# Kernel optimization log

Hardware: AMD Instinct MI355X
Metric: run time of the kernel (lower is better)

## Reference

```python
import jax, jax.numpy as jnp
import numpy as np

D_MODEL = 1024
NUM_HEADS = 16
D_K = D_MODEL // NUM_HEADS


def setup_inputs() -> dict:
    key = jax.random.key(0)
    ks = jax.random.split(key, 9)
    s = 1.0 / np.sqrt(D_MODEL)
    inp = {
        "x": jax.random.normal(ks[0], (2, 2048, D_MODEL), dtype=jnp.float32),
        "Wq": jax.random.uniform(ks[1], (D_MODEL, D_MODEL), jnp.float32, -s, s),
        "bq": jax.random.uniform(ks[2], (D_MODEL,), jnp.float32, -s, s),
        "Wk": jax.random.uniform(ks[3], (D_MODEL, D_MODEL), jnp.float32, -s, s),
        "bk": jax.random.uniform(ks[4], (D_MODEL,), jnp.float32, -s, s),
        "Wv": jax.random.uniform(ks[5], (D_MODEL, D_MODEL), jnp.float32, -s, s),
        "bv": jax.random.uniform(ks[6], (D_MODEL,), jnp.float32, -s, s),
        "Wo": jax.random.uniform(ks[7], (D_MODEL, D_MODEL), jnp.float32, -s, s),
        "bo": jax.random.uniform(ks[8], (D_MODEL,), jnp.float32, -s, s),
    }
    return inp


def reference(x, Wq, bq, Wk, bk, Wv, bv, Wo, bo):
    B, S, _ = x.shape
    # projections (torch Linear: y = x @ W.T + b)
    q = x @ Wq.T + bq
    k = x @ Wk.T + bk
    v = x @ Wv.T + bv
    # [B, H, S, Dk]
    q = q.reshape(B, S, NUM_HEADS, D_K).transpose(0, 2, 1, 3)
    k = k.reshape(B, S, NUM_HEADS, D_K).transpose(0, 2, 1, 3)
    v = v.reshape(B, S, NUM_HEADS, D_K).transpose(0, 2, 1, 3)
    scale = 1.0 / np.sqrt(D_K).astype(np.float32)
    energy = jnp.einsum("bhqd,bhkd->bhqk", q, k) * scale
    attn = jax.nn.softmax(energy, axis=-1)
    out = jnp.einsum("bhqk,bhkd->bhqd", attn, v)
    out = out.transpose(0, 2, 1, 3).reshape(B, S, D_MODEL)
    return out @ Wo.T + bo
```

## Files before the change

### kernel.cpp

```cpp
#include <hip/hip_runtime.h>
#include <hip/hip_bf16.h>
#include <cstdint>

typedef __bf16 bf16;
typedef __bf16 bf16x4 __attribute__((ext_vector_type(4)));
typedef __bf16 bf16x8 __attribute__((ext_vector_type(8)));
typedef float f32x4 __attribute__((ext_vector_type(4)));
typedef float f32x16 __attribute__((ext_vector_type(16)));
typedef unsigned int u32x4 __attribute__((ext_vector_type(4)));

#define DM   1024
#define SEQ  2048
#define NH   16
#define DKH  64

__device__ __forceinline__ bf16x8 ld8(const bf16* p) {
    return *reinterpret_cast<const bf16x8*>(p);
}

__device__ __forceinline__ void gld16(const void* g, void* lds) {
    __builtin_amdgcn_global_load_lds(
        (__attribute__((address_space(1))) void*)(uintptr_t)g,
        (__attribute__((address_space(3))) void*)(uint32_t)(uintptr_t)lds,
        16, 0, 0);
}

__device__ __forceinline__ f32x4 mfma16(bf16x8 a, bf16x8 b, f32x4 c) {
    return __builtin_amdgcn_mfma_f32_16x16x32_bf16(a, b, c, 0, 0, 0);
}
__device__ __forceinline__ f32x16 mfma32(bf16x8 a, bf16x8 b, f32x16 c) {
    return __builtin_amdgcn_mfma_f32_32x32x16_bf16(a, b, c, 0, 0, 0);
}

__device__ __forceinline__ unsigned pkbf(float lo, float hi) {
    unsigned r;
    asm("v_cvt_pk_bf16_f32 %0, %1, %2" : "=v"(r) : "v"(lo), "v"(hi));
    return r;
}
__device__ __forceinline__ void plswap(unsigned& a, unsigned& b) {
    asm volatile("v_permlane32_swap_b32 %0, %1" : "+v"(a), "+v"(b));
}

__global__ __launch_bounds__(256) void cvt_all(
    const float4* __restrict__ x,  const float4* __restrict__ wq,
    const float4* __restrict__ wk, const float4* __restrict__ wv,
    const float4* __restrict__ wo,
    ushort4* __restrict__ xb,  ushort4* __restrict__ wqb,
    ushort4* __restrict__ wkb, ushort4* __restrict__ wvb,
    ushort4* __restrict__ wob) {
    int i = blockIdx.x * 256 + threadIdx.x;
    const float4* src;
    ushort4* dst;
    int off;
    if (i < 1048576) {
        src = x; dst = xb; off = i;
    } else {
        int r = i - 1048576;
        int sel = r >> 18;
        off = r & 262143;
        src = sel == 0 ? wq : sel == 1 ? wk : sel == 2 ? wv : wo;
        dst = sel == 0 ? wqb : sel == 1 ? wkb : sel == 2 ? wvb : wob;
    }
    float4 f = src[off];
    ushort4 u;
    u.x = __builtin_bit_cast(unsigned short, (bf16)f.x);
    u.y = __builtin_bit_cast(unsigned short, (bf16)f.y);
    u.z = __builtin_bit_cast(unsigned short, (bf16)f.z);
    u.w = __builtin_bit_cast(unsigned short, (bf16)f.w);
    dst[off] = u;
}

template <int OUT_MODE>
__device__ __forceinline__ void gemm_body(const bf16* __restrict__ A,
                                          const bf16* __restrict__ W,
                                          const float* __restrict__ bias,
                                          void* __restrict__ outp,
                                          int m0, int n0, float scale,
                                          bf16* __restrict__ As,
                                          bf16* __restrict__ Bs) {
    constexpr int K = DM, BK = 64;

    const int t     = threadIdx.x;
    const int lane  = t & 63;
    const int row16 = lane & 15, grp = lane >> 4;
    const int wave  = t >> 6;
    const int wr    = (wave >> 1) * 64;
    const int wc    = (wave & 1) * 64;

    f32x4 acc[4][4] = {};

    const int sc = (t & 7) * 8;
    const bf16* Ag = A + (size_t)(m0 + (t >> 3)) * K + sc;
    const bf16* Wg = W + (size_t)(n0 + (t >> 3)) * K + sc;
    bf16* Asw = &As[t * 8];
    bf16* Bsw = &Bs[t * 8];

    for (int kt = 0; kt < K; kt += BK) {
        __syncthreads();
#pragma unroll
        for (int i = 0; i < 4; ++i) {
            gld16(Ag + (size_t)i * 32 * K + kt, Asw + i * 2048);
            gld16(Wg + (size_t)i * 32 * K + kt, Bsw + i * 2048);
        }
        __syncthreads();
#pragma unroll
        for (int kk = 0; kk < BK; kk += 32) {
            bf16x8 af[4], bfr[4];
#pragma unroll
            for (int m = 0; m < 4; ++m)
                af[m] = ld8(&As[(wr + m * 16 + row16) * BK + kk + grp * 8]);
#pragma unroll
            for (int n = 0; n < 4; ++n)
                bfr[n] = ld8(&Bs[(wc + n * 16 + row16) * BK + kk + grp * 8]);
#pragma unroll
            for (int m = 0; m < 4; ++m)
#pragma unroll
                for (int n = 0; n < 4; ++n)
                    acc[m][n] = mfma16(af[m], bfr[n], acc[m][n]);
        }
    }

    if constexpr (OUT_MODE == 2) {
        __syncthreads();
        bf16* Tw = (wave < 2) ? As + wave * 4096 : Bs + (wave - 2) * 4096;
        const int b = m0 >> 11;
        const int tokbase = (m0 & 2047) + wr;
#pragma unroll
        for (int n = 0; n < 4; ++n) {
            const int dim = n * 16 + row16;
            const float bv = bias[n0 + wc + dim];
#pragma unroll
            for (int m = 0; m < 4; ++m) {
                bf16x4 w4 = {(bf16)(acc[m][n][0] + bv), (bf16)(acc[m][n][1] + bv),
                             (bf16)(acc[m][n][2] + bv), (bf16)(acc[m][n][3] + bv)};
                const int slot = (m * 2 + (grp >> 1)) ^ (dim & 7);
                *reinterpret_cast<bf16x4*>(&Tw[dim * 64 + slot * 8 + (grp & 1) * 4]) = w4;
            }
        }
        asm volatile("" ::: "memory");
#pragma unroll
        for (int r = 0; r < 8; ++r) {
            const int dim = (lane >> 3) + 8 * r;
            const int ts  = lane & 7;
            bf16x8 v = ld8(&Tw[dim * 64 + ((ts ^ (dim & 7)) * 8)]);
            const int col = n0 + wc + dim;
            bf16* dst = (bf16*)outp +
                ((size_t)(b * NH + (col >> 6)) * DKH + (col & 63)) * SEQ +
                tokbase + ts * 8;
            *reinterpret_cast<bf16x8*>(dst) = v;
        }
    } else {
#pragma unroll
        for (int n = 0; n < 4; ++n) {
            const int col = n0 + wc + n * 16 + row16;
            const float bv = bias[col];
#pragma unroll
            for (int m = 0; m < 4; ++m) {
                const int row = m0 + wr + m * 16 + grp * 4;
#pragma unroll
                for (int j = 0; j < 4; ++j) {
                    float v = (acc[m][n][j] + bv) * scale;
                    if constexpr (OUT_MODE == 1)
                        ((float*)outp)[(size_t)(row + j) * DM + col] = v;
                    else
                        ((bf16*)outp)[(size_t)(row + j) * DM + col] = (bf16)v;
                }
            }
        }
    }
}

__global__ __launch_bounds__(256, 4) void gemm_qkv(
    const bf16* __restrict__ xb,
    const bf16* __restrict__ wqb, const bf16* __restrict__ wkb, const bf16* __restrict__ wvb,
    const float* __restrict__ bq, const float* __restrict__ bk, const float* __restrict__ bv,
    bf16* __restrict__ q, bf16* __restrict__ k, bf16* __restrict__ vt) {
    __shared__ __attribute__((aligned(16))) bf16 As[128 * 64];
    __shared__ __attribute__((aligned(16))) bf16 Bs[128 * 64];
    const int sel = blockIdx.y >> 3;
    const int m0 = blockIdx.x * 128, n0 = (blockIdx.y & 7) * 128;
    if (sel == 0) {
        gemm_body<0>(xb, wqb, bq, q, m0, n0, 0.18033688f, As, Bs);
    } else if (sel == 1) {
        gemm_body<0>(xb, wkb, bk, k, m0, n0, 1.0f, As, Bs);
    } else {
        gemm_body<2>(xb, wvb, bv, vt, m0, n0, 1.0f, As, Bs);
    }
}

__global__ __launch_bounds__(256, 4) void gemm_out(
    const bf16* __restrict__ ab, const bf16* __restrict__ wob,
    const float* __restrict__ bo, float* __restrict__ out) {
    __shared__ __attribute__((aligned(16))) bf16 As[128 * 64];
    __shared__ __attribute__((aligned(16))) bf16 Bs[128 * 64];
    gemm_body<1>(ab, wob, bo, out, blockIdx.x * 128, blockIdx.y * 128, 1.0f, As, Bs);
}

__global__ __launch_bounds__(256) void attn(const bf16* __restrict__ Q,
                                            const bf16* __restrict__ K,
                                            const bf16* __restrict__ VT,
                                            bf16* __restrict__ O) {
    __shared__ __attribute__((aligned(16))) bf16 Ks[2][64 * 64];
    __shared__ __attribute__((aligned(16))) bf16 Vs[2][64 * 64];

    const int t = threadIdx.x, lane = t & 63, wave = t >> 6;
    const int l31 = lane & 31, hi = lane >> 5;

    int id = blockIdx.x;
    id = (id & 7) * 64 + (id >> 3);
    const int qt = id & 15, h = (id >> 4) & 15, b = id >> 8;

    const bf16* Qb = Q + ((size_t)b * SEQ + qt * 128) * DM + h * DKH;
    const bf16* Kb = K + (size_t)b * SEQ * DM + h * DKH;
    const bf16* Vb = VT + (size_t)((b * NH + h) * DKH) * SEQ;

    bf16x8 qf[4];
#pragma unroll
    for (int c = 0; c < 4; ++c)
        qf[c] = ld8(Qb + (size_t)(wave * 32 + l31) * DM + c * 16 + hi * 8);

    f32x16 o[2] = {};
    float L = 0.f;

    const int sr = t >> 3, scs = t & 7;

    auto STAGE = [&](int bsel, int kt) {
#pragma unroll
        for (int i = 0; i < 2; ++i) {
            const int r = i * 32 + sr;
            const int cs = (scs ^ (r & 7)) * 8;
            gld16(Kb + (size_t)(kt + r) * DM + cs, &Ks[bsel][i * 2048 + t * 8]);
            gld16(Vb + (size_t)r * SEQ + kt + cs, &Vs[bsel][i * 2048 + t * 8]);
        }
    };

    STAGE(0, 0);
    __syncthreads();

    int cur = 0;
    for (int kt = 0; kt < SEQ; kt += 64) {
        if (kt + 64 < SEQ) STAGE(cur ^ 1, kt + 64);
        const bf16* KsB = Ks[cur];
        const bf16* VsB = Vs[cur];

        u32x4 up[4];
#pragma unroll
        for (int sub = 0; sub < 2; ++sub) {
            const int krow = sub * 32 + l31;
            const int ksw  = krow & 7;
            f32x16 ss = {};
            __builtin_amdgcn_s_setprio(1);
#pragma unroll
            for (int c = 0; c < 4; ++c) {
                const bf16x8 kf = ld8(&KsB[krow * 64 + (((c * 2 + hi) ^ ksw) * 8)]);
                ss = mfma32(kf, qf[c], ss);
            }
            __builtin_amdgcn_s_setprio(0);
            float e[16];
#pragma unroll
            for (int r = 0; r < 16; ++r) {
                e[r] = __builtin_amdgcn_exp2f(ss[r]);
                L += e[r];
            }
            unsigned u0 = pkbf(e[0],  e[1]),  u1 = pkbf(e[2],  e[3]);
            unsigned u2 = pkbf(e[4],  e[5]),  u3 = pkbf(e[6],  e[7]);
            unsigned u4 = pkbf(e[8],  e[9]),  u5 = pkbf(e[10], e[11]);
            unsigned u6 = pkbf(e[12], e[13]), u7 = pkbf(e[14], e[15]);
            plswap(u0, u2); plswap(u1, u3);
            plswap(u4, u6); plswap(u5, u7);
            up[sub * 2]     = u32x4{u0, u1, u2, u3};
            up[sub * 2 + 1] = u32x4{u4, u5, u6, u7};
        }

        __builtin_amdgcn_s_setprio(1);
#pragma unroll
        for (int dt = 0; dt < 2; ++dt) {
            const int vrow = dt * 32 + l31;
            const int vsw  = vrow & 7;
#pragma unroll
            for (int kc = 0; kc < 4; ++kc) {
                const bf16x8 vf = ld8(&VsB[vrow * 64 + (((kc * 2 + hi) ^ vsw) * 8)]);
                o[dt] = mfma32(__builtin_bit_cast(bf16x8, up[kc]), vf, o[dt]);
            }
        }
        __builtin_amdgcn_s_setprio(0);

        __syncthreads();
        cur ^= 1;
    }

    const float Lfull = L + __shfl_xor(L, 32);
    const float inv = 1.0f / Lfull;
    float invr[16];
#pragma unroll
    for (int r = 0; r < 16; ++r)
        invr[r] = __shfl(inv, (r & 3) + 8 * (r >> 2) + 4 * hi);
#pragma unroll
    for (int dt = 0; dt < 2; ++dt)
#pragma unroll
        for (int r = 0; r < 16; ++r) {
            const int ql = (r & 3) + 8 * (r >> 2) + 4 * hi;
            O[((size_t)b * SEQ + qt * 128 + wave * 32 + ql) * DM
              + h * DKH + dt * 32 + l31] = (bf16)(o[dt][r] * invr[r]);
        }
}

extern "C" void kernel_launch(void* const* d_in, const int* in_sizes, int n_in,
                              void* d_out, int out_size, void* d_ws, size_t ws_size,
                              hipStream_t stream) {
    const float* x  = (const float*)d_in[0];
    const float* Wq = (const float*)d_in[1];
    const float* bq = (const float*)d_in[2];
    const float* Wk = (const float*)d_in[3];
    const float* bk = (const float*)d_in[4];
    const float* Wv = (const float*)d_in[5];
    const float* bv = (const float*)d_in[6];
    const float* Wo = (const float*)d_in[7];
    const float* bo = (const float*)d_in[8];
    float* out = (float*)d_out;

    char* ws = (char*)d_ws;
    bf16* xb  = (bf16*)(ws + 0);
    bf16* wqb = (bf16*)(ws + 8388608);
    bf16* wkb = (bf16*)(ws + 10485760);
    bf16* wvb = (bf16*)(ws + 12582912);
    bf16* wob = (bf16*)(ws + 14680064);
    bf16* qb  = (bf16*)(ws + 16777216);
    bf16* kb  = (bf16*)(ws + 25165824);
    bf16* ab  = (bf16*)(ws + 33554432);
    bf16* vtb = (bf16*)(ws + 41943040);

    cvt_all<<<8192, 256, 0, stream>>>(
        (const float4*)x, (const float4*)Wq, (const float4*)Wk,
        (const float4*)Wv, (const float4*)Wo,
        (ushort4*)xb, (ushort4*)wqb, (ushort4*)wkb, (ushort4*)wvb, (ushort4*)wob);

    gemm_qkv<<<dim3(32, 24), 256, 0, stream>>>(xb, wqb, wkb, wvb, bq, bk, bv, qb, kb, vtb);

    attn<<<dim3(512), 256, 0, stream>>>(qb, kb, vtb, ab);

    gemm_out<<<dim3(32, 8), 256, 0, stream>>>(ab, wob, bo, out);
}
```

Before: 122.8 us.

## Rewrite QKV GEMM as 256x256 tile, double-buffered, swizzled LDS kernel

The fused QKV projection becomes a single 512-thread kernel with 256x256 output tiles over a concatenated Wq/Wk/Wv weight matrix, giving 192 blocks. Global-to-LDS loads are double-buffered with explicit vmcnt waits so the next K-tile's copy overlaps the current MFMAs. An XOR swizzle reduces LDS bank conflicts, and setprio raises priority around the MFMA block. The larger tile raises arithmetic intensity, but the 192-block grid may underfill the GPU's CUs and the kernel holds more registers and LDS per block.

```diff
diff --git a/kernel.cpp b/kernel.cpp
--- a/kernel.cpp
+++ b/kernel.cpp
@@ -70,15 +70,141 @@
     dst[off] = u;
 }
 
-template <int OUT_MODE>
-__device__ __forceinline__ void gemm_body(const bf16* __restrict__ A,
-                                          const bf16* __restrict__ W,
-                                          const float* __restrict__ bias,
-                                          void* __restrict__ outp,
-                                          int m0, int n0, float scale,
-                                          bf16* __restrict__ As,
-                                          bf16* __restrict__ Bs) {
+__global__ __launch_bounds__(512, 2) void gemm_qkv(
+    const bf16* __restrict__ A,
+    const bf16* __restrict__ W,
+    const float* __restrict__ bq, const float* __restrict__ bk,
+    const float* __restrict__ bv_,
+    bf16* __restrict__ q, bf16* __restrict__ k, bf16* __restrict__ vt) {
+    __shared__ __attribute__((aligned(16))) bf16 S[69632];
+
+    const int t    = threadIdx.x;
+    const int lane = t & 63;
+    const int r16  = lane & 15, grp = lane >> 4;
+    const int wave = t >> 6;
+    const int wr   = (wave >> 2) * 128;
+    const int wc   = (wave & 3) * 64;
+
+    int id = blockIdx.x;
+    id = (id & 7) * 24 + (id >> 3);
+    const int m0 = (id & 15) * 256;
+    const int n0 = (id >> 4) * 256;
+
+    f32x4 acc[8][4] = {};
+
+    const int srow = t >> 3;
+    const int scol = t & 7;
+
+    auto STAGE = [&](int buf, int kt) {
+#pragma unroll
+        for (int i = 0; i < 4; ++i) {
+            const int row = i * 64 + srow;
+            const int cs = ((scol ^ (row & 7)) * 8);
+            gld16(A + (size_t)(m0 + row) * DM + kt * 64 + cs,
+                  &S[buf * 32768 + i * 4096 + t * 8]);
+            gld16(W + (size_t)(n0 + row) * DM + kt * 64 + cs,
+                  &S[buf * 32768 + 16384 + i * 4096 + t * 8]);
+        }
+    };
+
+    STAGE(0, 0);
+    STAGE(1, 1);
+
+    for (int kt = 0; kt < 16; ++kt) {
+        if (kt == 15) { asm volatile("s_waitcnt vmcnt(0)" ::: "memory"); }
+        else         { asm volatile("s_waitcnt vmcnt(8)" ::: "memory"); }
+        __builtin_amdgcn_sched_barrier(0);
+        __builtin_amdgcn_s_barrier();
+
+        const int cur = kt & 1;
+        const bf16* Ab = &S[cur * 32768];
+        const bf16* Bb = &S[cur * 32768 + 16384];
+#pragma unroll
+        for (int kk = 0; kk < 2; ++kk) {
+            const int sl = kk * 4 + grp;
+            bf16x8 af[8], bf[4];
+#pragma unroll
+            for (int m = 0; m < 8; ++m) {
+                const int row = wr + m * 16 + r16;
+                af[m] = ld8(&Ab[row * 64 + ((sl ^ (row & 7)) * 8)]);
+            }
+#pragma unroll
+            for (int n = 0; n < 4; ++n) {
+                const int row = wc + n * 16 + r16;
+                bf[n] = ld8(&Bb[row * 64 + ((sl ^ (row & 7)) * 8)]);
+            }
+            __builtin_amdgcn_s_setprio(1);
+#pragma unroll
+            for (int m = 0; m < 8; ++m)
+#pragma unroll
+                for (int n = 0; n < 4; ++n)
+                    acc[m][n] = mfma16(af[m], bf[n], acc[m][n]);
+            __builtin_amdgcn_s_setprio(0);
+        }
+
+        __builtin_amdgcn_sched_barrier(0);
+        __builtin_amdgcn_s_barrier();
+        __builtin_amdgcn_sched_barrier(0);
+        if (kt + 2 < 16) STAGE(cur, kt + 2);
+    }
+
+    if (n0 < 2048) {
+        const float scale = (n0 < 1024) ? 0.18033688f : 1.0f;
+        bf16* out = (n0 < 1024) ? q : k;
+        const float* bias = (n0 < 1024) ? bq : bk;
+        const int nc0 = n0 & 1023;
+#pragma unroll
+        for (int n = 0; n < 4; ++n) {
+            const int col = nc0 + wc + n * 16 + r16;
+            const float bvv = bias[col];
+#pragma unroll
+            for (int m = 0; m < 8; ++m) {
+                const int row = m0 + wr + m * 16 + grp * 4;
+#pragma unroll
+                for (int j = 0; j < 4; ++j)
+                    out[(size_t)(row + j) * DM + col] =
+                        (bf16)((acc[m][n][j] + bvv) * scale);
+            }
+        }
+    } else {
+        const int nc0 = n0 - 2048;
+        const int b = m0 >> 11;
+        const int s0 = (m0 & 2047) + wr;
+        bf16* Tw = &S[wave * 8704];
+#pragma unroll
+        for (int n = 0; n < 4; ++n) {
+            const int dl = n * 16 + r16;
+            const float bvv = bv_[nc0 + wc + dl];
+#pragma unroll
+            for (int m = 0; m < 8; ++m) {
+                bf16x4 w4 = {(bf16)(acc[m][n][0] + bvv), (bf16)(acc[m][n][1] + bvv),
+                             (bf16)(acc[m][n][2] + bvv), (bf16)(acc[m][n][3] + bvv)};
+                *reinterpret_cast<bf16x4*>(&Tw[dl * 136 + m * 16 + grp * 4]) = w4;
+            }
+        }
+        asm volatile("" ::: "memory");
+#pragma unroll
+        for (int dd = 0; dd < 8; ++dd) {
+            const int dim = dd * 8 + (lane >> 3);
+            const int col = nc0 + wc + dim;
+            const int h = col >> 6, d = col & 63;
+            bf16* dst = vt + ((size_t)(b * NH + h) * DKH + d) * SEQ + s0;
+#pragma unroll
+            for (int cc = 0; cc < 2; ++cc) {
+                const int c = (lane & 7) + cc * 8;
+                bf16x8 v = ld8(&Tw[dim * 136 + c * 8]);
+                *reinterpret_cast<bf16x8*>(dst + c * 8) = v;
+            }
+        }
+    }
+}
+
+__global__ __launch_bounds__(256, 4) void gemm_out(
+    const bf16* __restrict__ A, const bf16* __restrict__ W,
+    const float* __restrict__ bias, float* __restrict__ out) {
     constexpr int K = DM, BK = 64;
+    __shared__ __attribute__((aligned(16))) bf16 As[128 * BK];
+    __shared__ __attribute__((aligned(16))) bf16 Bs[128 * BK];
 
     const int t     = threadIdx.x;
     const int lane  = t & 63;
@@ -86,6 +212,7 @@
     const int wave  = t >> 6;
     const int wr    = (wave >> 1) * 64;
     const int wc    = (wave & 1) * 64;
+    const int m0 = blockIdx.x * 128, n0 = blockIdx.y * 128;
 
     f32x4 acc[4][4] = {};
 
@@ -120,80 +247,18 @@
         }
     }
 
-    if constexpr (OUT_MODE == 2) {
-        __syncthreads();
-        bf16* Tw = (wave < 2) ? As + wave * 4096 : Bs + (wave - 2) * 4096;
-        const int b = m0 >> 11;
-        const int tokbase = (m0 & 2047) + wr;
-#pragma unroll
-        for (int n = 0; n < 4; ++n) {
-            const int dim = n * 16 + row16;
-            const float bv = bias[n0 + wc + dim];
-#pragma unroll
-            for (int m = 0; m < 4; ++m) {
-                bf16x4 w4 = {(bf16)(acc[m][n][0] + bv), (bf16)(acc[m][n][1] + bv),
-                             (bf16)(acc[m][n][2] + bv), (bf16)(acc[m][n][3] + bv)};
-                const int slot = (m * 2 + (grp >> 1)) ^ (dim & 7);
-                *reinterpret_cast<bf16x4*>(&Tw[dim * 64 + slot * 8 + (grp & 1) * 4]) = w4;
-            }
-        }
-        asm volatile("" ::: "memory");
-#pragma unroll
-        for (int r = 0; r < 8; ++r) {
-            const int dim = (lane >> 3) + 8 * r;
-            const int ts  = lane & 7;
-            bf16x8 v = ld8(&Tw[dim * 64 + ((ts ^ (dim & 7)) * 8)]);
-            const int col = n0 + wc + dim;
-            bf16* dst = (bf16*)outp +
-                ((size_t)(b * NH + (col >> 6)) * DKH + (col & 63)) * SEQ +
-                tokbase + ts * 8;
-            *reinterpret_cast<bf16x8*>(dst) = v;
-        }
-    } else {
-#pragma unroll
-        for (int n = 0; n < 4; ++n) {
-            const int col = n0 + wc + n * 16 + row16;
-            const float bv = bias[col];
-#pragma unroll
-            for (int m = 0; m < 4; ++m) {
-                const int row = m0 + wr + m * 16 + grp * 4;
-#pragma unroll
-                for (int j = 0; j < 4; ++j) {
-                    float v = (acc[m][n][j] + bv) * scale;
-                    if constexpr (OUT_MODE == 1)
-                        ((float*)outp)[(size_t)(row + j) * DM + col] = v;
-                    else
-                        ((bf16*)outp)[(size_t)(row + j) * DM + col] = (bf16)v;
-                }
-            }
-        }
-    }
-}
-
-__global__ __launch_bounds__(256, 4) void gemm_qkv(
-    const bf16* __restrict__ xb,
-    const bf16* __restrict__ wqb, const bf16* __restrict__ wkb, const bf16* __restrict__ wvb,
-    const float* __restrict__ bq, const float* __restrict__ bk, const float* __restrict__ bv,
-    bf16* __restrict__ q, bf16* __restrict__ k, bf16* __restrict__ vt) {
-    __shared__ __attribute__((aligned(16))) bf16 As[128 * 64];
-    __shared__ __attribute__((aligned(16))) bf16 Bs[128 * 64];
-    const int sel = blockIdx.y >> 3;
-    const int m0 = blockIdx.x * 128, n0 = (blockIdx.y & 7) * 128;
-    if (sel == 0) {
-        gemm_body<0>(xb, wqb, bq, q, m0, n0, 0.18033688f, As, Bs);
-    } else if (sel == 1) {
-        gemm_body<0>(xb, wkb, bk, k, m0, n0, 1.0f, As, Bs);
-    } else {
-        gemm_body<2>(xb, wvb, bv, vt, m0, n0, 1.0f, As, Bs);
-    }
-}
-
-__global__ __launch_bounds__(256, 4) void gemm_out(
-    const bf16* __restrict__ ab, const bf16* __restrict__ wob,
-    const float* __restrict__ bo, float* __restrict__ out) {
-    __shared__ __attribute__((aligned(16))) bf16 As[128 * 64];
-    __shared__ __attribute__((aligned(16))) bf16 Bs[128 * 64];
-    gemm_body<1>(ab, wob, bo, out, blockIdx.x * 128, blockIdx.y * 128, 1.0f, As, Bs);
+#pragma unroll
+    for (int n = 0; n < 4; ++n) {
+        const int col = n0 + wc + n * 16 + row16;
+        const float bvv = bias[col];
+#pragma unroll
+        for (int m = 0; m < 4; ++m) {
+            const int row = m0 + wr + m * 16 + grp * 4;
+#pragma unroll
+            for (int j = 0; j < 4; ++j)
+                out[(size_t)(row + j) * DM + col] = acc[m][n][j] + bvv;
+        }
+    }
 }
 
 __global__ __launch_bounds__(256) void attn(const bf16* __restrict__ Q,
@@ -320,22 +385,23 @@
     float* out = (float*)d_out;
 
     char* ws = (char*)d_ws;
-    bf16* xb  = (bf16*)(ws + 0);
-    bf16* wqb = (bf16*)(ws + 8388608);
-    bf16* wkb = (bf16*)(ws + 10485760);
-    bf16* wvb = (bf16*)(ws + 12582912);
-    bf16* wob = (bf16*)(ws + 14680064);
-    bf16* qb  = (bf16*)(ws + 16777216);
-    bf16* kb  = (bf16*)(ws + 25165824);
-    bf16* ab  = (bf16*)(ws + 33554432);
-    bf16* vtb = (bf16*)(ws + 41943040);
+    bf16* xb   = (bf16*)(ws + 0);
+    bf16* wqkv = (bf16*)(ws + 8388608);
+    bf16* wqb  = (bf16*)(ws + 8388608);
+    bf16* wkb  = (bf16*)(ws + 10485760);
+    bf16* wvb  = (bf16*)(ws + 12582912);
+    bf16* wob  = (bf16*)(ws + 14680064);
+    bf16* qb   = (bf16*)(ws + 16777216);
+    bf16* kb   = (bf16*)(ws + 25165824);
+    bf16* ab   = (bf16*)(ws + 33554432);
+    bf16* vtb  = (bf16*)(ws + 41943040);
 
     cvt_all<<<8192, 256, 0, stream>>>(
         (const float4*)x, (const float4*)Wq, (const float4*)Wk,
         (const float4*)Wv, (const float4*)Wo,
         (ushort4*)xb, (ushort4*)wqb, (ushort4*)wkb, (ushort4*)wvb, (ushort4*)wob);
 
-    gemm_qkv<<<dim3(32, 24), 256, 0, stream>>>(xb, wqb, wkb, wvb, bq, bk, bv, qb, kb, vtb);
+    gemm_qkv<<<192, 512, 0, stream>>>(xb, wqkv, bq, bk, bv, qb, kb, vtb);
 
     attn<<<dim3(512), 256, 0, stream>>>(qb, kb, vtb, ab);
 
```

Result: faster. 119.2 us (-2.9%).

## Triple-buffer GEMM K-loop with async LDS loads, swizzle and block remap

Applied to the files above, without the earlier changes.

Rewrites the shared GEMM body as a three-stage pipelined K-loop with BK=32. It uses global_load_lds prefetches two tiles ahead, partial vmcnt waits and a single barrier per step, so global loads overlap MFMA work. The LDS rows get an XOR swizzle against bank conflicts, and MFMA sections are wrapped in raised wave priority. The QKV GEMM now treats the contiguous Wq/Wk/Wv buffers as one fused weight matrix, and both GEMMs use a 1D grid with an XCD-aware block remap. The larger LDS footprint lowers the occupancy hint from 4 to 3 blocks per CU.

```diff
diff --git a/kernel.cpp b/kernel.cpp
--- a/kernel.cpp
+++ b/kernel.cpp
@@ -76,63 +76,80 @@
                                           const float* __restrict__ bias,
                                           void* __restrict__ outp,
                                           int m0, int n0, float scale,
-                                          bf16* __restrict__ As,
-                                          bf16* __restrict__ Bs) {
-    constexpr int K = DM, BK = 64;
-
-    const int t     = threadIdx.x;
-    const int lane  = t & 63;
-    const int row16 = lane & 15, grp = lane >> 4;
-    const int wave  = t >> 6;
-    const int wr    = (wave >> 1) * 64;
-    const int wc    = (wave & 1) * 64;
+                                          bf16* __restrict__ S) {
+    constexpr int BK = 32;
+    const int t    = threadIdx.x;
+    const int lane = t & 63;
+    const int r16  = lane & 15, grp = lane >> 4;
+    const int wave = t >> 6;
+    const int wr   = (wave >> 1) * 64;
+    const int wc   = (wave & 1) * 64;
 
     f32x4 acc[4][4] = {};
 
-    const int sc = (t & 7) * 8;
-    const bf16* Ag = A + (size_t)(m0 + (t >> 3)) * K + sc;
-    const bf16* Wg = W + (size_t)(n0 + (t >> 3)) * K + sc;
-    bf16* Asw = &As[t * 8];
-    bf16* Bsw = &Bs[t * 8];
-
-    for (int kt = 0; kt < K; kt += BK) {
-        __syncthreads();
-#pragma unroll
-        for (int i = 0; i < 4; ++i) {
-            gld16(Ag + (size_t)i * 32 * K + kt, Asw + i * 2048);
-            gld16(Wg + (size_t)i * 32 * K + kt, Bsw + i * 2048);
-        }
-        __syncthreads();
-#pragma unroll
-        for (int kk = 0; kk < BK; kk += 32) {
-            bf16x8 af[4], bfr[4];
-#pragma unroll
-            for (int m = 0; m < 4; ++m)
-                af[m] = ld8(&As[(wr + m * 16 + row16) * BK + kk + grp * 8]);
+    const int srow = t >> 2;
+    const int scol = t & 3;
+
+    auto STAGE = [&](int buf, int kt) {
+#pragma unroll
+        for (int i = 0; i < 2; ++i) {
+            const int row = i * 64 + srow;
+            const int cs = (scol ^ (row & 3)) * 8;
+            gld16(A + (size_t)(m0 + row) * DM + kt * BK + cs,
+                  &S[buf * 8192 + i * 2048 + t * 8]);
+            gld16(W + (size_t)(n0 + row) * DM + kt * BK + cs,
+                  &S[buf * 8192 + 4096 + i * 2048 + t * 8]);
+        }
+    };
+
+    STAGE(0, 0);
+    STAGE(1, 1);
+
+#pragma unroll
+    for (int kt = 0; kt < 32; ++kt) {
+        if (kt == 31) { asm volatile("s_waitcnt vmcnt(0)" ::: "memory"); }
+        else          { asm volatile("s_waitcnt vmcnt(4)" ::: "memory"); }
+        __builtin_amdgcn_sched_barrier(0);
+        __builtin_amdgcn_s_barrier();
+        __builtin_amdgcn_sched_barrier(0);
+
+        if (kt < 30) STAGE((kt + 2) % 3, kt + 2);
+
+        const bf16* Ab = &S[(kt % 3) * 8192];
+        const bf16* Bb = Ab + 4096;
+        bf16x8 af[4], bfr[4];
+#pragma unroll
+        for (int m = 0; m < 4; ++m) {
+            const int row = wr + m * 16 + r16;
+            af[m] = ld8(&Ab[row * BK + ((grp ^ (row & 3)) * 8)]);
+        }
+#pragma unroll
+        for (int n = 0; n < 4; ++n) {
+            const int row = wc + n * 16 + r16;
+            bfr[n] = ld8(&Bb[row * BK + ((grp ^ (row & 3)) * 8)]);
+        }
+        __builtin_amdgcn_s_setprio(1);
+#pragma unroll
+        for (int m = 0; m < 4; ++m)
 #pragma unroll
             for (int n = 0; n < 4; ++n)
-                bfr[n] = ld8(&Bs[(wc + n * 16 + row16) * BK + kk + grp * 8]);
-#pragma unroll
-            for (int m = 0; m < 4; ++m)
-#pragma unroll
-                for (int n = 0; n < 4; ++n)
-                    acc[m][n] = mfma16(af[m], bfr[n], acc[m][n]);
-        }
+                acc[m][n] = mfma16(af[m], bfr[n], acc[m][n]);
+        __builtin_amdgcn_s_setprio(0);
     }
 
     if constexpr (OUT_MODE == 2) {
         __syncthreads();
-        bf16* Tw = (wave < 2) ? As + wave * 4096 : Bs + (wave - 2) * 4096;
+        bf16* Tw = &S[wave * 4096];
         const int b = m0 >> 11;
         const int tokbase = (m0 & 2047) + wr;
 #pragma unroll
         for (int n = 0; n < 4; ++n) {
-            const int dim = n * 16 + row16;
-            const float bv = bias[n0 + wc + dim];
+            const int dim = n * 16 + r16;
+            const float bvv = bias[n0 - 2048 + wc + dim];
 #pragma unroll
             for (int m = 0; m < 4; ++m) {
-                bf16x4 w4 = {(bf16)(acc[m][n][0] + bv), (bf16)(acc[m][n][1] + bv),
-                             (bf16)(acc[m][n][2] + bv), (bf16)(acc[m][n][3] + bv)};
+                bf16x4 w4 = {(bf16)(acc[m][n][0] + bvv), (bf16)(acc[m][n][1] + bvv),
+                             (bf16)(acc[m][n][2] + bvv), (bf16)(acc[m][n][3] + bvv)};
                 const int slot = (m * 2 + (grp >> 1)) ^ (dim & 7);
                 *reinterpret_cast<bf16x4*>(&Tw[dim * 64 + slot * 8 + (grp & 1) * 4]) = w4;
             }
@@ -143,7 +160,7 @@
             const int dim = (lane >> 3) + 8 * r;
             const int ts  = lane & 7;
             bf16x8 v = ld8(&Tw[dim * 64 + ((ts ^ (dim & 7)) * 8)]);
-            const int col = n0 + wc + dim;
+            const int col = n0 - 2048 + wc + dim;
             bf16* dst = (bf16*)outp +
                 ((size_t)(b * NH + (col >> 6)) * DKH + (col & 63)) * SEQ +
                 tokbase + ts * 8;
@@ -152,14 +169,14 @@
     } else {
 #pragma unroll
         for (int n = 0; n < 4; ++n) {
-            const int col = n0 + wc + n * 16 + row16;
-            const float bv = bias[col];
+            const int col = (OUT_MODE == 0 ? (n0 & 1023) : n0) + wc + n * 16 + r16;
+            const float bvv = bias[col];
 #pragma unroll
             for (int m = 0; m < 4; ++m) {
                 const int row = m0 + wr + m * 16 + grp * 4;
 #pragma unroll
                 for (int j = 0; j < 4; ++j) {
-                    float v = (acc[m][n][j] + bv) * scale;
+                    float v = (acc[m][n][j] + bvv) * scale;
                     if constexpr (OUT_MODE == 1)
                         ((float*)outp)[(size_t)(row + j) * DM + col] = v;
                     else
@@ -170,30 +187,33 @@
     }
 }
 
-__global__ __launch_bounds__(256, 4) void gemm_qkv(
-    const bf16* __restrict__ xb,
-    const bf16* __restrict__ wqb, const bf16* __restrict__ wkb, const bf16* __restrict__ wvb,
-    const float* __restrict__ bq, const float* __restrict__ bk, const float* __restrict__ bv,
+__global__ __launch_bounds__(256, 3) void gemm_qkv(
+    const bf16* __restrict__ xb, const bf16* __restrict__ wqkv,
+    const float* __restrict__ bq, const float* __restrict__ bk,
+    const float* __restrict__ bv_,
     bf16* __restrict__ q, bf16* __restrict__ k, bf16* __restrict__ vt) {
-    __shared__ __attribute__((aligned(16))) bf16 As[128 * 64];
-    __shared__ __attribute__((aligned(16))) bf16 Bs[128 * 64];
-    const int sel = blockIdx.y >> 3;
-    const int m0 = blockIdx.x * 128, n0 = (blockIdx.y & 7) * 128;
-    if (sel == 0) {
-        gemm_body<0>(xb, wqb, bq, q, m0, n0, 0.18033688f, As, Bs);
-    } else if (sel == 1) {
-        gemm_body<0>(xb, wkb, bk, k, m0, n0, 1.0f, As, Bs);
+    __shared__ __attribute__((aligned(16))) bf16 S[24576];
+    int id = blockIdx.x;
+    id = (id & 7) * 96 + (id >> 3);
+    const int nt = id % 24, mt = id / 24;
+    const int m0 = mt * 128, n0 = nt * 128;
+    if (nt < 8) {
+        gemm_body<0>(xb, wqkv, bq, q, m0, n0, 0.18033688f, S);
+    } else if (nt < 16) {
+        gemm_body<0>(xb, wqkv, bk, k, m0, n0, 1.0f, S);
     } else {
-        gemm_body<2>(xb, wvb, bv, vt, m0, n0, 1.0f, As, Bs);
-    }
-}
-
-__global__ __launch_bounds__(256, 4) void gemm_out(
+        gemm_body<2>(xb, wqkv, bv_, vt, m0, n0, 1.0f, S);
+    }
+}
+
+__global__ __launch_bounds__(256, 3) void gemm_out(
     const bf16* __restrict__ ab, const bf16* __restrict__ wob,
     const float* __restrict__ bo, float* __restrict__ out) {
-    __shared__ __attribute__((aligned(16))) bf16 As[128 * 64];
-    __shared__ __attribute__((aligned(16))) bf16 Bs[128 * 64];
-    gemm_body<1>(ab, wob, bo, out, blockIdx.x * 128, blockIdx.y * 128, 1.0f, As, Bs);
+    __shared__ __attribute__((aligned(16))) bf16 S[24576];
+    int id = blockIdx.x;
+    id = (id & 7) * 32 + (id >> 3);
+    const int m0 = (id >> 3) * 128, n0 = (id & 7) * 128;
+    gemm_body<1>(ab, wob, bo, out, m0, n0, 1.0f, S);
 }
 
 __global__ __launch_bounds__(256) void attn(const bf16* __restrict__ Q,
@@ -320,24 +340,25 @@
     float* out = (float*)d_out;
 
     char* ws = (char*)d_ws;
-    bf16* xb  = (bf16*)(ws + 0);
-    bf16* wqb = (bf16*)(ws + 8388608);
-    bf16* wkb = (bf16*)(ws + 10485760);
-    bf16* wvb = (bf16*)(ws + 12582912);
-    bf16* wob = (bf16*)(ws + 14680064);
-    bf16* qb  = (bf16*)(ws + 16777216);
-    bf16* kb  = (bf16*)(ws + 25165824);
-    bf16* ab  = (bf16*)(ws + 33554432);
-    bf16* vtb = (bf16*)(ws + 41943040);
+    bf16* xb   = (bf16*)(ws + 0);
+    bf16* wqkv = (bf16*)(ws + 8388608);
+    bf16* wqb  = (bf16*)(ws + 8388608);
+    bf16* wkb  = (bf16*)(ws + 10485760);
+    bf16* wvb  = (bf16*)(ws + 12582912);
+    bf16* wob  = (bf16*)(ws + 14680064);
+    bf16* qb   = (bf16*)(ws + 16777216);
+    bf16* kb   = (bf16*)(ws + 25165824);
+    bf16* ab   = (bf16*)(ws + 33554432);
+    bf16* vtb  = (bf16*)(ws + 41943040);
 
     cvt_all<<<8192, 256, 0, stream>>>(
         (const float4*)x, (const float4*)Wq, (const float4*)Wk,
         (const float4*)Wv, (const float4*)Wo,
         (ushort4*)xb, (ushort4*)wqb, (ushort4*)wkb, (ushort4*)wvb, (ushort4*)wob);
 
-    gemm_qkv<<<dim3(32, 24), 256, 0, stream>>>(xb, wqb, wkb, wvb, bq, bk, bv, qb, kb, vtb);
+    gemm_qkv<<<768, 256, 0, stream>>>(xb, wqkv, bq, bk, bv, qb, kb, vtb);
 
     attn<<<dim3(512), 256, 0, stream>>>(qb, kb, vtb, ab);
 
-    gemm_out<<<dim3(32, 8), 256, 0, stream>>>(ab, wob, bo, out);
-}
+    gemm_out<<<256, 256, 0, stream>>>(ab, wob, bo, out);
+}
```

Measured after the change: 110.0 us. -10.4%, faster.
